# Optimization experiments

Measured on AMD Instinct MI355X. Metric: run time of the kernel, lower is better.

The kernel has to match this reference:

```python
import jax, jax.numpy as jnp
import numpy as np

H, N, OUT = 1024, 64, 512  # channels, SSM state size, output feats


def posenc3d(f, h, w, channels):
    # standard positional_encodings.PositionalEncoding3D
    ch = int(np.ceil(channels / 6) * 2)  # per-axis channels (342 for 1024)
    inv_freq = jnp.asarray(1.0 / (10000.0 ** (np.arange(0, ch, 2, dtype=np.float32) / ch)))

    def emb(n):
        s = jnp.arange(n, dtype=jnp.float32)[:, None] * inv_freq[None, :]  # (n, ch/2)
        return jnp.stack([jnp.sin(s), jnp.cos(s)], axis=-1).reshape(n, -1)  # interleaved (n, ch)

    ex, ey, ez = emb(f), emb(h), emb(w)
    pe = jnp.zeros((f, h, w, ch * 3), dtype=jnp.float32)
    pe = pe.at[..., :ch].set(ex[:, None, None, :])
    pe = pe.at[..., ch:2 * ch].set(ey[None, :, None, :])
    pe = pe.at[..., 2 * ch:].set(ez[None, None, :, :])
    return pe[..., :channels]  # truncate 3*342=1026 -> 1024


def s4_kernel(log_dt, A_re, A_im, C_re, C_im, L):
    # S4D ZOH kernel: K[h,l] = 2*Re( sum_n C'[h,n] * exp(dt_h*A[h,n]*l) )
    dt = jnp.exp(log_dt)                      # (H,)
    A = A_re + 1j * A_im                      # (H,N)
    C = C_re + 1j * C_im                      # (H,N)
    dtA = dt[:, None] * A                     # (H,N)
    Ct = C * (jnp.exp(dtA) - 1.0) / A         # discretized C' (H,N)
    l = jnp.arange(L, dtype=jnp.float32)

    def body(acc, xs):  # scan over state dim to avoid (H,N,L) materialization
        ct, da = xs  # (H,), (H,)
        return acc + ct[:, None] * jnp.exp(da[:, None] * l), None

    acc0 = jnp.zeros((log_dt.shape[0], L), dtype=jnp.complex64)
    K, _ = jax.lax.scan(body, acc0, (Ct.T, dtA.T))
    return 2.0 * K.real  # (H, L)


def reference(x, log_dt, A_re, A_im, C_re, C_im, D, W_out, b_out):
    bs, ch, f, h, w = x.shape
    L = f * h * w
    u = jnp.transpose(x, (0, 2, 3, 4, 1))                 # bs f h w ch
    u = u + posenc3d(f, h, w, ch)[None]
    u = u.reshape(bs, L, ch)
    v = jnp.transpose(u, (0, 2, 1))                       # (bs, ch, L)
    K = s4_kernel(log_dt, A_re, A_im, C_re, C_im, L)      # (ch, L)
    # causal FFT convolution (pad to 2L)
    Uf = jnp.fft.rfft(v, 2 * L)
    Kf = jnp.fft.rfft(K, 2 * L)
    y = jnp.fft.irfft(Uf * Kf[None], 2 * L)[..., :L]
    y = y + D[None, :, None] * v                          # skip connection
    y = jax.nn.gelu(jnp.transpose(y, (0, 2, 1)))          # (bs, L, ch)
    out = y @ W_out + b_out                               # (bs, L, OUT)
    return jnp.transpose(out, (0, 2, 1)).reshape(bs, W_out.shape[1], f, h, w)


def setup_inputs() -> dict:
    key = jax.random.key(0)
    ks = jax.random.split(key, 6)
    bs, f, h, w = 2, 16, 16, 16
    x = jax.random.normal(ks[0], (bs, H, f, h, w), dtype=jnp.float32)
    # S4D-Lin init
    log_dt = jax.random.uniform(ks[1], (H,), dtype=jnp.float32) * (np.log(0.1) - np.log(0.001)) + np.log(0.001)
    A_re = -0.5 * jnp.ones((H, N), dtype=jnp.float32)
    A_im = jnp.broadcast_to(np.pi * jnp.arange(N, dtype=jnp.float32)[None, :], (H, N)).copy()
    C_re = jax.random.normal(ks[2], (H, N), dtype=jnp.float32) * (0.5 ** 0.5)
    C_im = jax.random.normal(ks[3], (H, N), dtype=jnp.float32) * (0.5 ** 0.5)
    D = jax.random.normal(ks[4], (H,), dtype=jnp.float32)
    W_out = jax.random.normal(ks[5], (H, OUT), dtype=jnp.float32) / np.float32(np.sqrt(H))
    b_out = jnp.zeros((OUT,), dtype=jnp.float32)
    return {"x": x, "log_dt": log_dt, "A_re": A_re, "A_im": A_im, "C_re": C_re,
            "C_im": C_im, "D": D, "W_out": W_out, "b_out": b_out}
```

## Files before the change

kernel.cpp:

```cpp
#include <hip/hip_runtime.h>
#include <cstdint>
#include <cstddef>

#define H_CH 1024
#define OUTF 512
#define LSEQ 4096

typedef __bf16 bf16x8 __attribute__((ext_vector_type(8)));
typedef float floatx4 __attribute__((ext_vector_type(4)));

__device__ __forceinline__ unsigned short f2bf(float f) {
    __bf16 b = (__bf16)f;
    return __builtin_bit_cast(unsigned short, b);
}
__device__ __forceinline__ unsigned int pack2(float a, float b) {
    return (unsigned int)f2bf(a) | ((unsigned int)f2bf(b) << 16);
}
__device__ __forceinline__ float bf2f(unsigned short u) {
    unsigned int x = ((unsigned int)u) << 16;
    return __builtin_bit_cast(float, x);
}
struct c32 { float x, y; };
__device__ __forceinline__ c32 cmul(c32 a, c32 b) {
    return { fmaf(a.x, b.x, -a.y * b.y), fmaf(a.x, b.y, a.y * b.x) };
}
__device__ __forceinline__ c32 cpow16(c32 a, int w) {
    c32 p = {1.f, 0.f};
    if (w) {
        c32 a2 = cmul(a, a), a4 = cmul(a2, a2), a8 = cmul(a4, a4), a16 = cmul(a8, a8);
        p = a16;
        for (int k = 1; k < w; ++k) p = cmul(p, a16);
    }
    return p;
}

__global__ __launch_bounds__(256) void coef_kernel(
    const float* __restrict__ log_dt, const float* __restrict__ A_re,
    const float* __restrict__ A_im, const float* __restrict__ C_re,
    const float* __restrict__ C_im, float* __restrict__ coef)
{
    const int i = blockIdx.x * 256 + threadIdx.x;
    const int c = i >> 6;
    double are = A_re[i], aim = A_im[i], cre = C_re[i], cim = C_im[i];
    double dt  = exp((double)log_dt[c]);
    double dar = dt * are, dai = dt * aim;
    double er = exp(dar), cd = cos(dai), sd = sin(dai);
    double lre = er * cd, limm = er * sd;
    double ei = exp(-dar);
    double eQ = exp(64.0 * dar), cQ = cos(64.0 * dai), sQ = sin(64.0 * dai);
    double nre = lre - 1.0, nim = limm;
    double d2  = are * are + aim * aim;
    double qre = (nre * are + nim * aim) / d2;
    double qim = (nim * are - nre * aim) / d2;
    double ctre = cre * qre - cim * qim, ctim = cre * qim + cim * qre;
    float4 w0 = make_float4((float)lre, (float)limm, (float)(ei * cd), (float)(-ei * sd));
    float4 w1 = make_float4((float)(eQ * cQ), (float)(eQ * sQ),
                            (float)(2.0 * ctre), (float)(-2.0 * ctim));
    *(float4*)&coef[(size_t)i * 8]     = w0;
    *(float4*)&coef[(size_t)i * 8 + 4] = w1;
}

__global__ __launch_bounds__(256) void s4_fused_kernel(
    const float* __restrict__ x, const float* __restrict__ coef,
    const float* __restrict__ Dp, unsigned short* __restrict__ g)
{
    __shared__ __align__(16) unsigned short Vs[64 * 72];
    __shared__ __align__(16) unsigned short FP[128 * 72];
    __shared__ __align__(16) unsigned short Ss[64 * 136];
    __shared__ __align__(16) unsigned char  RY[64 * 136 * 2];
    __shared__ __align__(16) unsigned short Ts[64 * 72];
    __shared__ float2 Es[4][64];
    __shared__ float  pe16[16];
    unsigned short* Fs = FP;
    unsigned short* Ps = FP;
    unsigned short* Rs = (unsigned short*)RY;
    float* ytile = (float*)RY;

    const int wid = blockIdx.x;
    const int c = wid & (H_CH - 1);
    const int t = threadIdx.x, lane = t & 63, w = t >> 6, n = lane;
    const int lm = lane & 15, lq = lane >> 4;

    const int axis = (c >= 684) ? 2 : ((c >= 342) ? 1 : 0);
    const int j = c - 342 * axis;
    const int is_cos = j & 1;
    if (t < 16) {
        const float freq = (float)exp(-log(10000.0) * (double)(2 * (j >> 1)) / 342.0);
        float a = (float)t * freq;
        pe16[t] = is_cos ? cosf(a) : sinf(a);
    }

    const float* cf = coef + ((size_t)c * 64 + n) * 8;
    c32 lam = {cf[0], cf[1]}, inv = {cf[2], cf[3]}, lamQ = {cf[4], cf[5]};
    const float c2r = cf[6], c2mi = cf[7];
    const float Dc = Dp[c];
    __syncthreads();

    const float* xp = x + (size_t)wid * LSEQ;
    #pragma unroll
    for (int r = 0; r < 2; ++r) {
        const int i = r * 256 + t, l0 = i * 8;
        float4 f0 = *(const float4*)(xp + l0);
        float4 f1 = *(const float4*)(xp + l0 + 4);
        float e[8] = {f0.x, f0.y, f0.z, f0.w, f1.x, f1.y, f1.z, f1.w};
        unsigned int o[4];
        #pragma unroll
        for (int k = 0; k < 4; ++k) {
            const int la = l0 + 2 * k, lb = la + 1;
            const int pa = axis == 0 ? (la >> 8) : axis == 1 ? ((la >> 4) & 15) : (la & 15);
            const int pb = axis == 0 ? (lb >> 8) : axis == 1 ? ((lb >> 4) & 15) : (lb & 15);
            o[k] = pack2(e[2 * k] + pe16[pa], e[2 * k + 1] + pe16[pb]);
        }
        *(uint4*)&Vs[(i >> 3) * 72 + (i & 7) * 8] = make_uint4(o[0], o[1], o[2], o[3]);
    }
    {
        c32 l2 = cmul(lam, lam), l4 = cmul(l2, l2), l8 = cmul(l4, l4);
        c32 l16 = cmul(l8, l8), l32 = cmul(l16, l16);
        c32 z = cmul(cmul(cmul(cmul(cmul(l32, l16), l8), l4), l2), lam);
        z = cmul(z, cpow16(inv, w));
        #pragma unroll
        for (int s = 0; s < 16; ++s) {
            const int u = 16 * w + s;
            Fs[(2 * n) * 72 + u]     = f2bf(z.x);
            Fs[(2 * n + 1) * 72 + u] = f2bf(z.y);
            z = cmul(z, inv);
        }
    }
    __syncthreads();

    {
        floatx4 acc[2][4];
        #pragma unroll
        for (int a = 0; a < 2; ++a)
            #pragma unroll
            for (int b = 0; b < 4; ++b) acc[a][b] = (floatx4){0.f, 0.f, 0.f, 0.f};
        #pragma unroll
        for (int kt = 0; kt < 2; ++kt) {
            bf16x8 a0 = *(const bf16x8*)&Fs[(32 * w + lm) * 72 + kt * 32 + lq * 8];
            bf16x8 a1 = *(const bf16x8*)&Fs[(32 * w + 16 + lm) * 72 + kt * 32 + lq * 8];
            #pragma unroll
            for (int nt = 0; nt < 4; ++nt) {
                bf16x8 b = *(const bf16x8*)&Vs[(nt * 16 + lm) * 72 + kt * 32 + lq * 8];
                acc[0][nt] = __builtin_amdgcn_mfma_f32_16x16x32_bf16(a0, b, acc[0][nt], 0, 0, 0);
                acc[1][nt] = __builtin_amdgcn_mfma_f32_16x16x32_bf16(a1, b, acc[1][nt], 0, 0, 0);
            }
        }
        __syncthreads();
        #pragma unroll
        for (int sm = 0; sm < 2; ++sm)
            #pragma unroll
            for (int nt = 0; nt < 4; ++nt) {
                const int row = 32 * w + sm * 16 + lq * 4, col = nt * 16 + lm;
                *(uint2*)&Ss[col * 136 + row] =
                    make_uint2(pack2(acc[sm][nt][0], acc[sm][nt][1]),
                               pack2(acc[sm][nt][2], acc[sm][nt][3]));
            }
    }
    __syncthreads();

    {
        c32 z = cmul((c32){c2r, -c2mi}, cpow16(lam, w));
        const int steps = (w == 3) ? 17 : 16;
        for (int s = 0; s < steps; ++s) {
            const int tt = 16 * w + s;
            *(unsigned int*)&Ps[tt * 136 + 2 * n] = pack2(z.x, -z.y);
            z = cmul(z, lam);
        }
    }
    {
        c32 z = cpow16(inv, w);
        #pragma unroll
        for (int s = 0; s < 16; ++s) {
            const int u = 16 * w + s;
            *(unsigned int*)&Rs[u * 136 + 2 * n] = pack2(z.x, z.y);
            z = cmul(z, inv);
        }
    }
    {
        float sr = 0.f, si = 0.f;
        #pragma unroll
        for (int jc = 0; jc < 16; ++jc) {
            unsigned int d = *(unsigned int*)&Ss[(16 * w + jc) * 136 + 2 * n];
            float dr = bf2f((unsigned short)(d & 0xffff));
            float di = bf2f((unsigned short)(d >> 16));
            float nr = fmaf(lamQ.x, sr, fmaf(-lamQ.y, si, dr));
            float ni = fmaf(lamQ.x, si, fmaf(lamQ.y, sr, di));
            sr = nr; si = ni;
        }
        Es[w][n] = make_float2(sr, si);
    }
    __syncthreads();

    {
        c32 Q2 = cmul(lamQ, lamQ), Q4 = cmul(Q2, Q2), Q8 = cmul(Q4, Q4);
        c32 Q16 = cmul(Q8, Q8);
        float cr = 0.f, ci = 0.f;
        for (int w2 = 0; w2 < w; ++w2) {
            float2 e = Es[w2][n];
            float nr = fmaf(Q16.x, cr, fmaf(-Q16.y, ci, e.x));
            float ni = fmaf(Q16.x, ci, fmaf(Q16.y, cr, e.y));
            cr = nr; ci = ni;
        }
        float sr = cr, si = ci;
        #pragma unroll
        for (int jc = 0; jc < 16; ++jc) {
            unsigned int* p = (unsigned int*)&Ss[(16 * w + jc) * 136 + 2 * n];
            unsigned int d = *p;
            *p = pack2(sr, si);
            float dr = bf2f((unsigned short)(d & 0xffff));
            float di = bf2f((unsigned short)(d >> 16));
            float nr = fmaf(lamQ.x, sr, fmaf(-lamQ.y, si, dr));
            float ni = fmaf(lamQ.x, si, fmaf(lamQ.y, sr, di));
            sr = nr; si = ni;
        }
    }
    __syncthreads();

    {
        floatx4 a1[4];
        #pragma unroll
        for (int nt = 0; nt < 4; ++nt) a1[nt] = (floatx4){0.f, 0.f, 0.f, 0.f};
        #pragma unroll
        for (int kt = 0; kt < 4; ++kt) {
            bf16x8 a = *(const bf16x8*)&Ps[(16 * w + lm) * 136 + kt * 32 + lq * 8];
            #pragma unroll
            for (int nt = 0; nt < 4; ++nt) {
                bf16x8 b = *(const bf16x8*)&Rs[(nt * 16 + lm) * 136 + kt * 32 + lq * 8];
                a1[nt] = __builtin_amdgcn_mfma_f32_16x16x32_bf16(a, b, a1[nt], 0, 0, 0);
            }
        }
        #pragma unroll
        for (int nt = 0; nt < 4; ++nt)
            #pragma unroll
            for (int r = 0; r < 4; ++r) {
                const int row = 16 * w + lq * 4 + r, col = nt * 16 + lm;
                Ts[row * 72 + col] = f2bf(row >= col ? a1[nt][r] : 0.f);
            }
    }
    __syncthreads();

    {
        floatx4 a2[4];
        #pragma unroll
        for (int nt = 0; nt < 4; ++nt) a2[nt] = (floatx4){0.f, 0.f, 0.f, 0.f};
        #pragma unroll
        for (int kt = 0; kt < 2; ++kt) {
            bf16x8 a = *(const bf16x8*)&Ts[(16 * w + lm) * 72 + kt * 32 + lq * 8];
            #pragma unroll
            for (int nt = 0; nt < 4; ++nt) {
                bf16x8 b = *(const bf16x8*)&Vs[(nt * 16 + lm) * 72 + kt * 32 + lq * 8];
                a2[nt] = __builtin_amdgcn_mfma_f32_16x16x32_bf16(a, b, a2[nt], 0, 0, 0);
            }
        }
        #pragma unroll
        for (int kt = 0; kt < 4; ++kt) {
            bf16x8 a = *(const bf16x8*)&Ps[(16 * w + lm + 1) * 136 + kt * 32 + lq * 8];
            #pragma unroll
            for (int nt = 0; nt < 4; ++nt) {
                bf16x8 b = *(const bf16x8*)&Ss[(nt * 16 + lm) * 136 + kt * 32 + lq * 8];
                a2[nt] = __builtin_amdgcn_mfma_f32_16x16x32_bf16(a, b, a2[nt], 0, 0, 0);
            }
        }
        #pragma unroll
        for (int nt = 0; nt < 4; ++nt)
            #pragma unroll
            for (int r = 0; r < 4; ++r) {
                const int tt = 16 * w + lq * 4 + r, chunk = nt * 16 + lm;
                const float vv = bf2f(Vs[chunk * 72 + tt]);
                const float y = fmaf(Dc, vv, a2[nt][r]);
                const float u = y + 0.044715f * y * y * y;
                const float gg = 0.5f * y * (1.f + tanhf(0.7978845608028654f * u));
                ytile[chunk * 68 + tt] = gg;
            }
    }
    __syncthreads();
    unsigned int* gp = (unsigned int*)(g + (size_t)wid * LSEQ);
    #pragma unroll
    for (int q = 0; q < 8; ++q) {
        const int idx = q * 256 + t, l = idx * 2;
        const int ch = l >> 6, tt = l & 63;
        gp[idx] = pack2(ytile[ch * 68 + tt], ytile[ch * 68 + tt + 1]);
    }
}

__global__ __launch_bounds__(256) void transpose_g_kernel(
    const unsigned short* __restrict__ g_bcl, unsigned short* __restrict__ gT)
{
    __shared__ unsigned int tileU[64 * 33];
    const int t = threadIdx.x, ty = t >> 5, tx = t & 31;
    const int l0 = blockIdx.x * 64, c0 = blockIdx.y * 64, b = blockIdx.z;
    #pragma unroll
    for (int r = 0; r < 8; ++r) {
        const int ci = r * 8 + ty;
        tileU[ci * 33 + tx] =
            *(const unsigned int*)&g_bcl[((size_t)b * H_CH + c0 + ci) * LSEQ + l0 + tx * 2];
    }
    __syncthreads();
    #pragma unroll
    for (int r = 0; r < 8; ++r) {
        const int li = r * 8 + ty;
        unsigned int ua = tileU[(2 * tx) * 33 + (li >> 1)];
        unsigned int ub = tileU[(2 * tx + 1) * 33 + (li >> 1)];
        unsigned int s0 = (li & 1) ? (ua >> 16) : (ua & 0xffffu);
        unsigned int s1 = (li & 1) ? (ub >> 16) : (ub & 0xffffu);
        *(unsigned int*)&gT[((size_t)b * LSEQ + l0 + li) * H_CH + c0 + 2 * tx] =
            s0 | (s1 << 16);
    }
}

__global__ __launch_bounds__(256) void transpose_w_kernel(
    const float* __restrict__ W, unsigned short* __restrict__ Wt)
{
    __shared__ float tileF[64 * 65];
    const int t = threadIdx.x;
    const int o0 = blockIdx.x * 64, k0 = blockIdx.y * 64;
    {
        const int ty = t >> 6, tx = t & 63;
        #pragma unroll
        for (int r = 0; r < 16; ++r) {
            const int ki = r * 4 + ty;
            tileF[ki * 65 + tx] = W[(size_t)(k0 + ki) * OUTF + o0 + tx];
        }
    }
    __syncthreads();
    {
        const int ty = t >> 5, tx = t & 31;
        #pragma unroll
        for (int r = 0; r < 8; ++r) {
            const int oi = r * 8 + ty;
            unsigned int u0 = f2bf(tileF[(2 * tx) * 65 + oi]);
            unsigned int u1 = f2bf(tileF[(2 * tx + 1) * 65 + oi]);
            *(unsigned int*)&Wt[(size_t)(o0 + oi) * H_CH + k0 + 2 * tx] = u0 | (u1 << 16);
        }
    }
}

__global__ __launch_bounds__(256) void gemm_kernel(
    const unsigned short* __restrict__ gT, const unsigned short* __restrict__ Wt,
    const float* __restrict__ b_out, float* __restrict__ out)
{
    __shared__ unsigned short As[64 * 40];
    __shared__ unsigned short Bs[128 * 40];
    const int t = threadIdx.x, lane = t & 63, w = t >> 6;
    const int lm = lane & 15, lq = lane >> 4;
    const int l0 = blockIdx.x * 128, o0 = blockIdx.y * 64, bb = blockIdx.z;
    const unsigned short* gB = gT + (size_t)bb * LSEQ * H_CH;

    floatx4 acc[4][2];
    #pragma unroll
    for (int i = 0; i < 4; ++i)
        #pragma unroll
        for (int jj = 0; jj < 2; ++jj) acc[i][jj] = (floatx4){0.f, 0.f, 0.f, 0.f};

    for (int kt = 0; kt < 32; ++kt) {
        const int k0 = kt * 32;
        __syncthreads();
        {
            const int row = t >> 2, q = t & 3;
            *(uint4*)&As[row * 40 + q * 8] =
                *(const uint4*)(Wt + (size_t)(o0 + row) * H_CH + k0 + q * 8);
        }
        #pragma unroll
        for (int half = 0; half < 2; ++half) {
            const int chunk = t + half * 256, row = chunk >> 2, q = chunk & 3;
            *(uint4*)&Bs[row * 40 + q * 8] =
                *(const uint4*)(gB + (size_t)(l0 + row) * H_CH + k0 + q * 8);
        }
        __syncthreads();

        bf16x8 af[4], bfr[2];
        #pragma unroll
        for (int sm = 0; sm < 4; ++sm)
            af[sm] = *(const bf16x8*)&As[(sm * 16 + lm) * 40 + lq * 8];
        #pragma unroll
        for (int sn = 0; sn < 2; ++sn)
            bfr[sn] = *(const bf16x8*)&Bs[(w * 32 + sn * 16 + lm) * 40 + lq * 8];
        #pragma unroll
        for (int sm = 0; sm < 4; ++sm)
            #pragma unroll
            for (int sn = 0; sn < 2; ++sn)
                acc[sm][sn] = __builtin_amdgcn_mfma_f32_16x16x32_bf16(
                    af[sm], bfr[sn], acc[sm][sn], 0, 0, 0);
    }
    #pragma unroll
    for (int sm = 0; sm < 4; ++sm)
        #pragma unroll
        for (int sn = 0; sn < 2; ++sn)
            #pragma unroll
            for (int r = 0; r < 4; ++r) {
                const int o = o0 + sm * 16 + lq * 4 + r;
                const int l = l0 + w * 32 + sn * 16 + lm;
                out[((size_t)bb * OUTF + o) * LSEQ + l] = acc[sm][sn][r] + b_out[o];
            }
}

extern "C" void kernel_launch(void* const* d_in, const int* in_sizes, int n_in,
                              void* d_out, int out_size, void* d_ws, size_t ws_size,
                              hipStream_t stream) {
    const float* x      = (const float*)d_in[0];
    const float* log_dt = (const float*)d_in[1];
    const float* A_re   = (const float*)d_in[2];
    const float* A_im   = (const float*)d_in[3];
    const float* C_re   = (const float*)d_in[4];
    const float* C_im   = (const float*)d_in[5];
    const float* Dp     = (const float*)d_in[6];
    const float* W_out  = (const float*)d_in[7];
    const float* b_out  = (const float*)d_in[8];
    float* out = (float*)d_out;

    char* ws = (char*)d_ws;
    unsigned short* g    = (unsigned short*)ws;
    unsigned short* gT   = (unsigned short*)(ws + (size_t)16 * 1024 * 1024);
    unsigned short* Wt   = (unsigned short*)(ws + (size_t)32 * 1024 * 1024);
    float*          coef = (float*)(ws + (size_t)33 * 1024 * 1024);

    coef_kernel<<<256, 256, 0, stream>>>(log_dt, A_re, A_im, C_re, C_im, coef);
    s4_fused_kernel<<<2048, 256, 0, stream>>>(x, coef, Dp, g);
    transpose_g_kernel<<<dim3(64, 16, 2), 256, 0, stream>>>(g, gT);
    transpose_w_kernel<<<dim3(8, 16), 256, 0, stream>>>(W_out, Wt);
    gemm_kernel<<<dim3(32, 8, 2), 256, 0, stream>>>(gT, Wt, b_out, out);
}
```

Measured before the change: 157.0 us.

## Process both batches per channel block, enlarge GEMM tile, use fast GELU

The S4 fused kernel now runs one block per channel and handles both batch elements, so the per-channel P/T/R factor setup is computed once and reused across the batch. The GELU tanh is replaced by an exp/rcp sigmoid form, and output packing writes bf16 pairs straight into shared memory. The final GEMM tile grows to 128x128 per block with 4x4 MFMA accumulators per wave, which raises operand reuse. The trade-offs are half as many blocks in the fused kernel, more registers in the GEMM, and a slightly different GELU approximation.

Measured after the change: 147.7 us. -6.0%, faster.

```diff
diff --git a/kernel.cpp b/kernel.cpp
--- a/kernel.cpp
+++ b/kernel.cpp
@@ -32,6 +32,11 @@
         for (int k = 1; k < w; ++k) p = cmul(p, a16);
     }
     return p;
+}
+__device__ __forceinline__ float gelu_fast(float y) {
+    float u = y + 0.044715f * y * y * y;
+    float e = __expf(-1.5957691216057308f * u);
+    return y * __builtin_amdgcn_rcpf(1.f + e);
 }
 
 __global__ __launch_bounds__(256) void coef_kernel(
@@ -65,19 +70,17 @@
     const float* __restrict__ Dp, unsigned short* __restrict__ g)
 {
     __shared__ __align__(16) unsigned short Vs[64 * 72];
-    __shared__ __align__(16) unsigned short FP[128 * 72];
+    __shared__ __align__(16) unsigned short Ps[65 * 136];
+    __shared__ __align__(16) unsigned char  RY[128 * 72 * 2];
     __shared__ __align__(16) unsigned short Ss[64 * 136];
-    __shared__ __align__(16) unsigned char  RY[64 * 136 * 2];
     __shared__ __align__(16) unsigned short Ts[64 * 72];
     __shared__ float2 Es[4][64];
     __shared__ float  pe16[16];
-    unsigned short* Fs = FP;
-    unsigned short* Ps = FP;
-    unsigned short* Rs = (unsigned short*)RY;
-    float* ytile = (float*)RY;
-
-    const int wid = blockIdx.x;
-    const int c = wid & (H_CH - 1);
+    unsigned short* Fs   = (unsigned short*)RY;
+    unsigned short* Rs   = (unsigned short*)RY;
+    unsigned int*   ybuf = (unsigned int*)RY;
+
+    const int c = blockIdx.x;
     const int t = threadIdx.x, lane = t & 63, w = t >> 6, n = lane;
     const int lm = lane & 15, lq = lane >> 4;
 
@@ -89,74 +92,160 @@
         float a = (float)t * freq;
         pe16[t] = is_cos ? cosf(a) : sinf(a);
     }
-
     const float* cf = coef + ((size_t)c * 64 + n) * 8;
     c32 lam = {cf[0], cf[1]}, inv = {cf[2], cf[3]}, lamQ = {cf[4], cf[5]};
     const float c2r = cf[6], c2mi = cf[7];
     const float Dc = Dp[c];
     __syncthreads();
 
-    const float* xp = x + (size_t)wid * LSEQ;
-    #pragma unroll
-    for (int r = 0; r < 2; ++r) {
-        const int i = r * 256 + t, l0 = i * 8;
-        float4 f0 = *(const float4*)(xp + l0);
-        float4 f1 = *(const float4*)(xp + l0 + 4);
-        float e[8] = {f0.x, f0.y, f0.z, f0.w, f1.x, f1.y, f1.z, f1.w};
-        unsigned int o[4];
-        #pragma unroll
-        for (int k = 0; k < 4; ++k) {
-            const int la = l0 + 2 * k, lb = la + 1;
-            const int pa = axis == 0 ? (la >> 8) : axis == 1 ? ((la >> 4) & 15) : (la & 15);
-            const int pb = axis == 0 ? (lb >> 8) : axis == 1 ? ((lb >> 4) & 15) : (lb & 15);
-            o[k] = pack2(e[2 * k] + pe16[pa], e[2 * k + 1] + pe16[pb]);
-        }
-        *(uint4*)&Vs[(i >> 3) * 72 + (i & 7) * 8] = make_uint4(o[0], o[1], o[2], o[3]);
-    }
-    {
-        c32 l2 = cmul(lam, lam), l4 = cmul(l2, l2), l8 = cmul(l4, l4);
-        c32 l16 = cmul(l8, l8), l32 = cmul(l16, l16);
-        c32 z = cmul(cmul(cmul(cmul(cmul(l32, l16), l8), l4), l2), lam);
-        z = cmul(z, cpow16(inv, w));
-        #pragma unroll
-        for (int s = 0; s < 16; ++s) {
-            const int u = 16 * w + s;
-            Fs[(2 * n) * 72 + u]     = f2bf(z.x);
-            Fs[(2 * n + 1) * 72 + u] = f2bf(z.y);
-            z = cmul(z, inv);
-        }
-    }
-    __syncthreads();
-
-    {
-        floatx4 acc[2][4];
-        #pragma unroll
-        for (int a = 0; a < 2; ++a)
-            #pragma unroll
-            for (int b = 0; b < 4; ++b) acc[a][b] = (floatx4){0.f, 0.f, 0.f, 0.f};
+    auto deltascan = [&](int bb) {
+        const float* xp = x + ((size_t)bb * H_CH + c) * (size_t)LSEQ;
+        #pragma unroll
+        for (int r = 0; r < 2; ++r) {
+            const int i = r * 256 + t, l0 = i * 8;
+            float4 f0 = *(const float4*)(xp + l0);
+            float4 f1 = *(const float4*)(xp + l0 + 4);
+            float e[8] = {f0.x, f0.y, f0.z, f0.w, f1.x, f1.y, f1.z, f1.w};
+            unsigned int o[4];
+            #pragma unroll
+            for (int k = 0; k < 4; ++k) {
+                const int la = l0 + 2 * k, lb = la + 1;
+                const int pa = axis == 0 ? (la >> 8) : axis == 1 ? ((la >> 4) & 15) : (la & 15);
+                const int pb = axis == 0 ? (lb >> 8) : axis == 1 ? ((lb >> 4) & 15) : (lb & 15);
+                o[k] = pack2(e[2 * k] + pe16[pa], e[2 * k + 1] + pe16[pb]);
+            }
+            *(uint4*)&Vs[(i >> 3) * 72 + (i & 7) * 8] = make_uint4(o[0], o[1], o[2], o[3]);
+        }
+        {
+            c32 l2 = cmul(lam, lam), l4 = cmul(l2, l2), l8 = cmul(l4, l4);
+            c32 l16 = cmul(l8, l8), l32 = cmul(l16, l16);
+            c32 z = cmul(cmul(cmul(cmul(cmul(l32, l16), l8), l4), l2), lam);
+            z = cmul(z, cpow16(inv, w));
+            #pragma unroll
+            for (int s = 0; s < 16; ++s) {
+                const int u = 16 * w + s;
+                Fs[(2 * n) * 72 + u]     = f2bf(z.x);
+                Fs[(2 * n + 1) * 72 + u] = f2bf(z.y);
+                z = cmul(z, inv);
+            }
+        }
+        __syncthreads();
+        {
+            floatx4 acc[2][4];
+            #pragma unroll
+            for (int a = 0; a < 2; ++a)
+                #pragma unroll
+                for (int b = 0; b < 4; ++b) acc[a][b] = (floatx4){0.f, 0.f, 0.f, 0.f};
+            #pragma unroll
+            for (int kt = 0; kt < 2; ++kt) {
+                bf16x8 a0 = *(const bf16x8*)&Fs[(32 * w + lm) * 72 + kt * 32 + lq * 8];
+                bf16x8 a1 = *(const bf16x8*)&Fs[(32 * w + 16 + lm) * 72 + kt * 32 + lq * 8];
+                #pragma unroll
+                for (int nt = 0; nt < 4; ++nt) {
+                    bf16x8 b = *(const bf16x8*)&Vs[(nt * 16 + lm) * 72 + kt * 32 + lq * 8];
+                    acc[0][nt] = __builtin_amdgcn_mfma_f32_16x16x32_bf16(a0, b, acc[0][nt], 0, 0, 0);
+                    acc[1][nt] = __builtin_amdgcn_mfma_f32_16x16x32_bf16(a1, b, acc[1][nt], 0, 0, 0);
+                }
+            }
+            #pragma unroll
+            for (int sm = 0; sm < 2; ++sm)
+                #pragma unroll
+                for (int nt = 0; nt < 4; ++nt) {
+                    const int row = 32 * w + sm * 16 + lq * 4, col = nt * 16 + lm;
+                    *(uint2*)&Ss[col * 136 + row] =
+                        make_uint2(pack2(acc[sm][nt][0], acc[sm][nt][1]),
+                                   pack2(acc[sm][nt][2], acc[sm][nt][3]));
+                }
+        }
+        __syncthreads();
+        {
+            float sr = 0.f, si = 0.f;
+            #pragma unroll
+            for (int jc = 0; jc < 16; ++jc) {
+                unsigned int d = *(unsigned int*)&Ss[(16 * w + jc) * 136 + 2 * n];
+                float dr = bf2f((unsigned short)(d & 0xffff));
+                float di = bf2f((unsigned short)(d >> 16));
+                float nr = fmaf(lamQ.x, sr, fmaf(-lamQ.y, si, dr));
+                float ni = fmaf(lamQ.x, si, fmaf(lamQ.y, sr, di));
+                sr = nr; si = ni;
+            }
+            Es[w][n] = make_float2(sr, si);
+        }
+        __syncthreads();
+        {
+            c32 Q2 = cmul(lamQ, lamQ), Q4 = cmul(Q2, Q2), Q8 = cmul(Q4, Q4);
+            c32 Q16 = cmul(Q8, Q8);
+            float cr = 0.f, ci = 0.f;
+            for (int w2 = 0; w2 < w; ++w2) {
+                float2 e = Es[w2][n];
+                float nr = fmaf(Q16.x, cr, fmaf(-Q16.y, ci, e.x));
+                float ni = fmaf(Q16.x, ci, fmaf(Q16.y, cr, e.y));
+                cr = nr; ci = ni;
+            }
+            float sr = cr, si = ci;
+            #pragma unroll
+            for (int jc = 0; jc < 16; ++jc) {
+                unsigned int* p = (unsigned int*)&Ss[(16 * w + jc) * 136 + 2 * n];
+                unsigned int d = *p;
+                *p = pack2(sr, si);
+                float dr = bf2f((unsigned short)(d & 0xffff));
+                float di = bf2f((unsigned short)(d >> 16));
+                float nr = fmaf(lamQ.x, sr, fmaf(-lamQ.y, si, dr));
+                float ni = fmaf(lamQ.x, si, fmaf(lamQ.y, sr, di));
+                sr = nr; si = ni;
+            }
+        }
+        __syncthreads();
+    };
+
+    auto gemm2_epi = [&](int bb) {
+        floatx4 a2[4];
+        #pragma unroll
+        for (int nt = 0; nt < 4; ++nt) a2[nt] = (floatx4){0.f, 0.f, 0.f, 0.f};
         #pragma unroll
         for (int kt = 0; kt < 2; ++kt) {
-            bf16x8 a0 = *(const bf16x8*)&Fs[(32 * w + lm) * 72 + kt * 32 + lq * 8];
-            bf16x8 a1 = *(const bf16x8*)&Fs[(32 * w + 16 + lm) * 72 + kt * 32 + lq * 8];
+            bf16x8 a = *(const bf16x8*)&Ts[(16 * w + lm) * 72 + kt * 32 + lq * 8];
             #pragma unroll
             for (int nt = 0; nt < 4; ++nt) {
                 bf16x8 b = *(const bf16x8*)&Vs[(nt * 16 + lm) * 72 + kt * 32 + lq * 8];
-                acc[0][nt] = __builtin_amdgcn_mfma_f32_16x16x32_bf16(a0, b, acc[0][nt], 0, 0, 0);
-                acc[1][nt] = __builtin_amdgcn_mfma_f32_16x16x32_bf16(a1, b, acc[1][nt], 0, 0, 0);
-            }
-        }
-        __syncthreads();
-        #pragma unroll
-        for (int sm = 0; sm < 2; ++sm)
+                a2[nt] = __builtin_amdgcn_mfma_f32_16x16x32_bf16(a, b, a2[nt], 0, 0, 0);
+            }
+        }
+        #pragma unroll
+        for (int kt = 0; kt < 4; ++kt) {
+            bf16x8 a = *(const bf16x8*)&Ps[(16 * w + lm + 1) * 136 + kt * 32 + lq * 8];
             #pragma unroll
             for (int nt = 0; nt < 4; ++nt) {
-                const int row = 32 * w + sm * 16 + lq * 4, col = nt * 16 + lm;
-                *(uint2*)&Ss[col * 136 + row] =
-                    make_uint2(pack2(acc[sm][nt][0], acc[sm][nt][1]),
-                               pack2(acc[sm][nt][2], acc[sm][nt][3]));
-            }
-    }
-    __syncthreads();
+                bf16x8 b = *(const bf16x8*)&Ss[(nt * 16 + lm) * 136 + kt * 32 + lq * 8];
+                a2[nt] = __builtin_amdgcn_mfma_f32_16x16x32_bf16(a, b, a2[nt], 0, 0, 0);
+            }
+        }
+        __syncthreads();
+        #pragma unroll
+        for (int nt = 0; nt < 4; ++nt) {
+            const int chunk = nt * 16 + lm;
+            float gg[4];
+            #pragma unroll
+            for (int r = 0; r < 4; ++r) {
+                const int tt = 16 * w + lq * 4 + r;
+                const float vv = bf2f(Vs[chunk * 72 + tt]);
+                gg[r] = gelu_fast(fmaf(Dc, vv, a2[nt][r]));
+            }
+            const int p0 = 8 * w + 2 * lq;
+            ybuf[chunk * 34 + p0]     = pack2(gg[0], gg[1]);
+            ybuf[chunk * 34 + p0 + 1] = pack2(gg[2], gg[3]);
+        }
+        __syncthreads();
+        unsigned int* gp = (unsigned int*)(g + ((size_t)bb * H_CH + c) * (size_t)LSEQ);
+        #pragma unroll
+        for (int q = 0; q < 8; ++q) {
+            const int idx = q * 256 + t;
+            gp[idx] = ybuf[(idx >> 5) * 34 + (idx & 31)];
+        }
+        __syncthreads();
+    };
+
+    deltascan(0);
 
     {
         c32 z = cmul((c32){c2r, -c2mi}, cpow16(lam, w));
@@ -176,46 +265,7 @@
             z = cmul(z, inv);
         }
     }
-    {
-        float sr = 0.f, si = 0.f;
-        #pragma unroll
-        for (int jc = 0; jc < 16; ++jc) {
-            unsigned int d = *(unsigned int*)&Ss[(16 * w + jc) * 136 + 2 * n];
-            float dr = bf2f((unsigned short)(d & 0xffff));
-            float di = bf2f((unsigned short)(d >> 16));
-            float nr = fmaf(lamQ.x, sr, fmaf(-lamQ.y, si, dr));
-            float ni = fmaf(lamQ.x, si, fmaf(lamQ.y, sr, di));
-            sr = nr; si = ni;
-        }
-        Es[w][n] = make_float2(sr, si);
-    }
     __syncthreads();
-
-    {
-        c32 Q2 = cmul(lamQ, lamQ), Q4 = cmul(Q2, Q2), Q8 = cmul(Q4, Q4);
-        c32 Q16 = cmul(Q8, Q8);
-        float cr = 0.f, ci = 0.f;
-        for (int w2 = 0; w2 < w; ++w2) {
-            float2 e = Es[w2][n];
-            float nr = fmaf(Q16.x, cr, fmaf(-Q16.y, ci, e.x));
-            float ni = fmaf(Q16.x, ci, fmaf(Q16.y, cr, e.y));
-            cr = nr; ci = ni;
-        }
-        float sr = cr, si = ci;
-        #pragma unroll
-        for (int jc = 0; jc < 16; ++jc) {
-            unsigned int* p = (unsigned int*)&Ss[(16 * w + jc) * 136 + 2 * n];
-            unsigned int d = *p;
-            *p = pack2(sr, si);
-            float dr = bf2f((unsigned short)(d & 0xffff));
-            float di = bf2f((unsigned short)(d >> 16));
-            float nr = fmaf(lamQ.x, sr, fmaf(-lamQ.y, si, dr));
-            float ni = fmaf(lamQ.x, si, fmaf(lamQ.y, sr, di));
-            sr = nr; si = ni;
-        }
-    }
-    __syncthreads();
-
     {
         floatx4 a1[4];
         #pragma unroll
@@ -239,48 +289,9 @@
     }
     __syncthreads();
 
-    {
-        floatx4 a2[4];
-        #pragma unroll
-        for (int nt = 0; nt < 4; ++nt) a2[nt] = (floatx4){0.f, 0.f, 0.f, 0.f};
-        #pragma unroll
-        for (int kt = 0; kt < 2; ++kt) {
-            bf16x8 a = *(const bf16x8*)&Ts[(16 * w + lm) * 72 + kt * 32 + lq * 8];
-            #pragma unroll
-            for (int nt = 0; nt < 4; ++nt) {
-                bf16x8 b = *(const bf16x8*)&Vs[(nt * 16 + lm) * 72 + kt * 32 + lq * 8];
-                a2[nt] = __builtin_amdgcn_mfma_f32_16x16x32_bf16(a, b, a2[nt], 0, 0, 0);
-            }
-        }
-        #pragma unroll
-        for (int kt = 0; kt < 4; ++kt) {
-            bf16x8 a = *(const bf16x8*)&Ps[(16 * w + lm + 1) * 136 + kt * 32 + lq * 8];
-            #pragma unroll
-            for (int nt = 0; nt < 4; ++nt) {
-                bf16x8 b = *(const bf16x8*)&Ss[(nt * 16 + lm) * 136 + kt * 32 + lq * 8];
-                a2[nt] = __builtin_amdgcn_mfma_f32_16x16x32_bf16(a, b, a2[nt], 0, 0, 0);
-            }
-        }
-        #pragma unroll
-        for (int nt = 0; nt < 4; ++nt)
-            #pragma unroll
-            for (int r = 0; r < 4; ++r) {
-                const int tt = 16 * w + lq * 4 + r, chunk = nt * 16 + lm;
-                const float vv = bf2f(Vs[chunk * 72 + tt]);
-                const float y = fmaf(Dc, vv, a2[nt][r]);
-                const float u = y + 0.044715f * y * y * y;
-                const float gg = 0.5f * y * (1.f + tanhf(0.7978845608028654f * u));
-                ytile[chunk * 68 + tt] = gg;
-            }
-    }
-    __syncthreads();
-    unsigned int* gp = (unsigned int*)(g + (size_t)wid * LSEQ);
-    #pragma unroll
-    for (int q = 0; q < 8; ++q) {
-        const int idx = q * 256 + t, l = idx * 2;
-        const int ch = l >> 6, tt = l & 63;
-        gp[idx] = pack2(ytile[ch * 68 + tt], ytile[ch * 68 + tt + 1]);
-    }
+    gemm2_epi(0);
+    deltascan(1);
+    gemm2_epi(1);
 }
 
 __global__ __launch_bounds__(256) void transpose_g_kernel(
@@ -339,57 +350,57 @@
     const unsigned short* __restrict__ gT, const unsigned short* __restrict__ Wt,
     const float* __restrict__ b_out, float* __restrict__ out)
 {
-    __shared__ unsigned short As[64 * 40];
+    __shared__ unsigned short As[128 * 40];
     __shared__ unsigned short Bs[128 * 40];
-    const int t = threadIdx.x, lane = t & 63, w = t >> 6;
+    const int t = threadIdx.x, lane = t & 63, wid = t >> 6;
+    const int wo = wid & 1, wl = wid >> 1;
     const int lm = lane & 15, lq = lane >> 4;
-    const int l0 = blockIdx.x * 128, o0 = blockIdx.y * 64, bb = blockIdx.z;
+    const int l0 = blockIdx.x * 128, o0 = blockIdx.y * 128, bb = blockIdx.z;
     const unsigned short* gB = gT + (size_t)bb * LSEQ * H_CH;
 
-    floatx4 acc[4][2];
+    floatx4 acc[4][4];
     #pragma unroll
     for (int i = 0; i < 4; ++i)
         #pragma unroll
-        for (int jj = 0; jj < 2; ++jj) acc[i][jj] = (floatx4){0.f, 0.f, 0.f, 0.f};
+        for (int jj = 0; jj < 4; ++jj) acc[i][jj] = (floatx4){0.f, 0.f, 0.f, 0.f};
 
     for (int kt = 0; kt < 32; ++kt) {
         const int k0 = kt * 32;
         __syncthreads();
-        {
-            const int row = t >> 2, q = t & 3;
+        #pragma unroll
+        for (int half = 0; half < 2; ++half) {
+            const int chunk = t + half * 256;
+            const int row = chunk >> 2, q = chunk & 3;
             *(uint4*)&As[row * 40 + q * 8] =
                 *(const uint4*)(Wt + (size_t)(o0 + row) * H_CH + k0 + q * 8);
-        }
-        #pragma unroll
-        for (int half = 0; half < 2; ++half) {
-            const int chunk = t + half * 256, row = chunk >> 2, q = chunk & 3;
             *(uint4*)&Bs[row * 40 + q * 8] =
                 *(const uint4*)(gB + (size_t)(l0 + row) * H_CH + k0 + q * 8);
         }
         __syncthreads();
 
-        bf16x8 af[4], bfr[2];
+        bf16x8 af[4], bfr[4];
         #pragma unroll
         for (int sm = 0; sm < 4; ++sm)
-            af[sm] = *(const bf16x8*)&As[(sm * 16 + lm) * 40 + lq * 8];
-        #pragma unroll
-        for (int sn = 0; sn < 2; ++sn)
-            bfr[sn] = *(const bf16x8*)&Bs[(w * 32 + sn * 16 + lm) * 40 + lq * 8];
+            af[sm] = *(const bf16x8*)&As[(wo * 64 + sm * 16 + lm) * 40 + lq * 8];
+        #pragma unroll
+        for (int sn = 0; sn < 4; ++sn)
+            bfr[sn] = *(const bf16x8*)&Bs[(wl * 64 + sn * 16 + lm) * 40 + lq * 8];
         #pragma unroll
         for (int sm = 0; sm < 4; ++sm)
             #pragma unroll
-            for (int sn = 0; sn < 2; ++sn)
+            for (int sn = 0; sn < 4; ++sn)
                 acc[sm][sn] = __builtin_amdgcn_mfma_f32_16x16x32_bf16(
                     af[sm], bfr[sn], acc[sm][sn], 0, 0, 0);
     }
+
     #pragma unroll
     for (int sm = 0; sm < 4; ++sm)
         #pragma unroll
-        for (int sn = 0; sn < 2; ++sn)
+        for (int sn = 0; sn < 4; ++sn)
             #pragma unroll
             for (int r = 0; r < 4; ++r) {
-                const int o = o0 + sm * 16 + lq * 4 + r;
-                const int l = l0 + w * 32 + sn * 16 + lm;
+                const int o = o0 + wo * 64 + sm * 16 + lq * 4 + r;
+                const int l = l0 + wl * 64 + sn * 16 + lm;
                 out[((size_t)bb * OUTF + o) * LSEQ + l] = acc[sm][sn][r] + b_out[o];
             }
 }
@@ -415,8 +426,8 @@
     float*          coef = (float*)(ws + (size_t)33 * 1024 * 1024);
 
     coef_kernel<<<256, 256, 0, stream>>>(log_dt, A_re, A_im, C_re, C_im, coef);
-    s4_fused_kernel<<<2048, 256, 0, stream>>>(x, coef, Dp, g);
+    s4_fused_kernel<<<1024, 256, 0, stream>>>(x, coef, Dp, g);
     transpose_g_kernel<<<dim3(64, 16, 2), 256, 0, stream>>>(g, gT);
     transpose_w_kernel<<<dim3(8, 16), 256, 0, stream>>>(W_out, Wt);
-    gemm_kernel<<<dim3(32, 8, 2), 256, 0, stream>>>(gT, Wt, b_out, out);
-}
+    gemm_kernel<<<dim3(32, 4, 2), 256, 0, stream>>>(gT, Wt, b_out, out);
+}
```
